# Kernel tuning notes

Measured on AMD Instinct MI355X. Metric: run time of the kernel, lower is better.

The kernel has to match this reference:

```python
import jax, jax.numpy as jnp
import numpy as np

K = 3          # kernel_size
P = 1          # padding
S = 1          # stride
C_IN = 64
C_OUT = 64


def unfold_patches(t, k=K, p=P, s=S):
    """Replicate-pad then extract kxk patches.
    Input  t: [B, C, H, W]
    Output  : [B, Ho, Wo, C, k*k]  matching torch unfold(2).unfold(3).permute(0,2,3,1,4,5).reshape
    (patch index varies as kh*k + kw)."""
    B, C, H, W = t.shape
    tp = jnp.pad(t, ((0, 0), (0, 0), (p, p), (p, p)), mode='edge')
    Ho = (H + 2 * p - k) // s + 1
    Wo = (W + 2 * p - k) // s + 1
    pats = [tp[:, :, a:a + (Ho - 1) * s + 1:s, b:b + (Wo - 1) * s + 1:s]
            for a in range(k) for b in range(k)]
    y = jnp.stack(pats, axis=-1)          # [B, C, Ho, Wo, k*k]
    return jnp.transpose(y, (0, 2, 3, 1, 4))  # [B, Ho, Wo, C, k*k]


def setup_inputs() -> dict:
    key = jax.random.key(0)
    k1, k2, k3, k4, k5, k6, k7 = jax.random.split(key, 7)
    B, H, W = 4, 128, 128
    feat_in = K * K * C_IN * 2      # 1152
    f1_out = K * K * C_IN           # 576
    f2_out = C_IN * C_OUT           # 4096
    lim1 = 1.0 / np.sqrt(feat_in)
    x = jax.random.normal(k1, (B, C_IN, H, W), dtype=jnp.float32)
    m = jax.random.uniform(k2, (B, C_IN, H, W), dtype=jnp.float32)
    s = jax.random.uniform(k3, (B, C_IN, H, W), dtype=jnp.float32)
    W1 = jax.random.uniform(k4, (feat_in, f1_out), minval=-lim1, maxval=lim1, dtype=jnp.float32)
    b1 = jax.random.uniform(k5, (f1_out,), minval=-lim1, maxval=lim1, dtype=jnp.float32)
    W2 = jax.random.uniform(k6, (feat_in, f2_out), minval=-lim1, maxval=lim1, dtype=jnp.float32)
    b2 = jax.random.uniform(k7, (f2_out,), minval=-lim1, maxval=lim1, dtype=jnp.float32)
    return {"x": x, "m": m, "s": s, "W1": W1, "b1": b1, "W2": W2, "b2": b2}


def reference(x, m, s, W1, b1, W2, b2):
    yp = unfold_patches(x)                              # [B,Ho,Wo,Cin,K2]
    mp = jax.lax.stop_gradient(unfold_patches(m))       # torch no_grad
    sp = jax.lax.stop_gradient(unfold_patches(s))
    B, Ho, Wo = yp.shape[:3]

    feat = jnp.concatenate([yp.reshape(B, Ho, Wo, -1),
                            mp.reshape(B, Ho, Wo, -1)], axis=-1)  # [B,Ho,Wo,2*K2*Cin]
    w1 = (feat @ W1 + b1).reshape(B, Ho, Wo, C_IN, K * K)
    w2 = (feat @ W2 + b2).reshape(B, Ho, Wo, C_IN, C_OUT)

    # y = sum_c (sum_k yp*w1) * w2
    yr = jnp.einsum('bhwck,bhwck->bhwc', yp, w1)
    y = jnp.einsum('bhwc,bhwco->bhwo', yr, w2)
    y = jnp.transpose(y, (0, 3, 1, 2))                  # [B,Cout,Ho,Wo]

    aw1 = jnp.abs(w1)
    aw2 = jnp.abs(w2)
    mr = jnp.einsum('bhwck,bhwck->bhwc', mp, aw1)
    m_y = jnp.transpose(jnp.einsum('bhwc,bhwco->bhwo', mr, aw2), (0, 3, 1, 2))
    sr = jnp.einsum('bhwck,bhwck->bhwc', sp, aw1)
    s_y = jnp.transpose(jnp.einsum('bhwc,bhwco->bhwo', sr, aw2), (0, 3, 1, 2))
    m_y = jax.lax.stop_gradient(m_y / s_y)

    return (y, m_y, jnp.ones_like(m_y))
```

## Files before the change

### kernel.cpp

```cpp
#include <hip/hip_runtime.h>
#include <stdint.h>
#include <stddef.h>


using short8   = __attribute__((ext_vector_type(8))) short;
using float4v  = __attribute__((ext_vector_type(4))) float;
using ushort4v = __attribute__((ext_vector_type(4))) unsigned short;

#define DI __device__ __forceinline__

DI unsigned short f2bf(float f) {
  union { float f; unsigned int u; } a; a.f = f;
  unsigned int r = a.u + 0x7fffu + ((a.u >> 16) & 1u);
  return (unsigned short)(r >> 16);
}
DI float bf2f(unsigned short u) {
  union { unsigned int u; float f; } a; a.u = ((unsigned int)u) << 16;
  return a.f;
}
DI void gll16(const void* g, void* l) {
  __builtin_amdgcn_global_load_lds(
      (const __attribute__((address_space(1))) unsigned int*)g,
      (__attribute__((address_space(3))) unsigned int*)l, 16, 0, 0);
}

__global__ void k_feat(const float* __restrict__ x, const float* __restrict__ m,
                       unsigned short* __restrict__ featb) {
  unsigned int tid = blockIdx.x * 256u + threadIdx.x;
  int j8   = tid & 7;
  int pl   = (tid >> 3) & 127;
  int q    = (tid >> 10) & 3;
  int pblk = (tid >> 12) & 511;
  int kk   = tid >> 21;
  int col  = kk * 32 + q * 8 + j8;
  const float* src = x;
  int jx = col;
  if (col >= 576) { src = m; jx = col - 576; }
  int c  = jx / 9;
  int t  = jx - c * 9;
  int t3 = t / 3;
  int dh = t3 - 1;
  int dw = (t - t3 * 3) - 1;
  int p  = pblk * 128 + pl;
  int b  = p >> 14, h = (p >> 7) & 127, w = p & 127;
  int hh = min(max(h + dh, 0), 127);
  int ww = min(max(w + dw, 0), 127);
  featb[tid] = f2bf(src[(((b << 6) | c) << 14) + (hh << 7) + ww]);
}

__global__ void k_sw(const float* __restrict__ Wsrc, unsigned short* __restrict__ Wdst,
                     int ncols, int ntiles, int total, int perm) {
  int tid = blockIdx.x * 256 + threadIdx.x;
  if (tid >= total) return;
  int k = tid / ncols;
  int n = tid - k * ncols;
  int np = perm ? (((n & 63) << 6) | (n >> 6)) : n;
  int out = ((k >> 5) * ntiles + (np >> 4)) * 512 + ((k >> 3) & 3) * 128 +
            (np & 15) * 8 + (k & 7);
  Wdst[out] = f2bf(Wsrc[tid]);
}

__launch_bounds__(512, 2)
__global__ void k_gemm1(const unsigned short* __restrict__ featb,
                        const unsigned short* __restrict__ W1s,
                        const float* __restrict__ b1,
                        const float* __restrict__ x, const float* __restrict__ m,
                        const float* __restrict__ s,
                        float* __restrict__ yr, float* __restrict__ mr,
                        float* __restrict__ sr) {
  __shared__ __align__(16) unsigned short Alds[4096];
  __shared__ __align__(16) unsigned short Blds[4608];
  __shared__ __align__(16) unsigned short w1buf[128 * 152];
  const int tid = threadIdx.x;
  const int wv  = tid >> 6;
  const int l15 = tid & 15;
  const int q   = (tid >> 4) & 3;
  const int bm  = blockIdx.x, nb = blockIdx.y;

  float4v acc[9];
#pragma unroll
  for (int t = 0; t < 9; ++t) acc[t] = (float4v){0.f, 0.f, 0.f, 0.f};

  const unsigned short* Ab = featb + (size_t)bm * 4096;
  const unsigned short* Bb = W1s + (size_t)nb * 9 * 512;

  for (int kk = 0; kk < 36; ++kk) {
    __syncthreads();
    gll16(Ab + (size_t)kk * 2097152 + tid * 8, (char*)Alds + wv * 1024);
    gll16(Bb + (size_t)kk * 18432 + tid * 8, (char*)Blds + wv * 1024);
    if (tid < 64) gll16(Bb + (size_t)kk * 18432 + 4096 + tid * 8, (char*)Blds + 8192);
    __syncthreads();
    short8 af = *(const short8*)&Alds[q * 1024 + (16 * wv + l15) * 8];
#pragma unroll
    for (int t = 0; t < 9; ++t) {
      short8 bfr = *(const short8*)&Blds[t * 512 + q * 128 + l15 * 8];
      acc[t] = __builtin_amdgcn_mfma_f32_16x16x32_bf16(af, bfr, acc[t], 0, 0, 0);
    }
  }

#pragma unroll
  for (int t = 0; t < 9; ++t) {
    int col = 16 * t + l15;
    float bb = b1[nb * 144 + col];
#pragma unroll
    for (int i = 0; i < 4; ++i) {
      int plr = 16 * wv + 4 * q + i;
      w1buf[plr * 152 + col] = f2bf(acc[t][i] + bb);
    }
  }
  __syncthreads();

  const int b = bm >> 7, h = bm & 127;
#pragma unroll
  for (int ii = 0; ii < 4; ++ii) {
    int task = ii * 512 + tid;
    int p  = task >> 4;
    int cl = task & 15;
    int c  = nb * 16 + cl;
    float w1v[9];
#pragma unroll
    for (int k = 0; k < 9; ++k) w1v[k] = bf2f(w1buf[p * 152 + cl * 9 + k]);
    size_t base = (size_t)(((b << 6) | c) << 14);
    float vy = 0.f, vm = 0.f, vs = 0.f;
#pragma unroll
    for (int dh = -1; dh <= 1; ++dh) {
      int hh = min(max(h + dh, 0), 127);
#pragma unroll
      for (int dw = -1; dw <= 1; ++dw) {
        int ww = min(max(p + dw, 0), 127);
        size_t idx = base + (hh << 7) + ww;
        int k = (dh + 1) * 3 + (dw + 1);
        float wv1 = w1v[k], aw = fabsf(wv1);
        vy += x[idx] * wv1;
        vm += m[idx] * aw;
        vs += s[idx] * aw;
      }
    }
    size_t P = (size_t)bm * 128 + p;
    yr[P * 64 + c] = vy;
    mr[P * 64 + c] = vm;
    sr[P * 64 + c] = vs;
  }
}

__launch_bounds__(512, 2)
__global__ void k_gemm2(const unsigned short* __restrict__ featb,
                        const unsigned short* __restrict__ W2s,
                        const float* __restrict__ b2,
                        const float* __restrict__ yr, const float* __restrict__ mr,
                        const float* __restrict__ sr,
                        float* __restrict__ out) {
  __shared__ __align__(16) unsigned short U[3][16384];
  __shared__ __align__(16) unsigned short w2buf[256 * 68];
  const int tid  = threadIdx.x;
  const int wv   = tid >> 6;
  const int lane = tid & 63;
  const int wm   = wv >> 2;
  const int wn   = wv & 3;
  const int l15  = tid & 15;
  const int q    = (tid >> 4) & 3;
  const int part = lane >> 4;
  const int bm   = blockIdx.x;

  const unsigned short* Ab = featb + (size_t)bm * 8192;

  float4v acc[8][4];
#pragma unroll
  for (int r = 0; r < 8; ++r)
#pragma unroll
    for (int t = 0; t < 4; ++t) acc[r][t] = (float4v){0.f, 0.f, 0.f, 0.f};

  gll16(Ab + tid * 8,                  (char*)&U[0][0]     + wv * 1024);
  gll16(Ab + 4096 + tid * 8,           (char*)&U[0][4096]  + wv * 1024);
  gll16(W2s + tid * 8,                 (char*)&U[0][8192]  + wv * 1024);
  gll16(W2s + 4096 + tid * 8,          (char*)&U[0][12288] + wv * 1024);
  gll16(Ab + 2097152 + tid * 8,        (char*)&U[1][0]     + wv * 1024);
  gll16(Ab + 2097152 + 4096 + tid * 8, (char*)&U[1][4096]  + wv * 1024);
  gll16(W2s + 131072 + tid * 8,        (char*)&U[1][8192]  + wv * 1024);
  gll16(W2s + 131072 + 4096 + tid * 8, (char*)&U[1][12288] + wv * 1024);

#define G2_STEP(KK, BR, BS, LAST)                                              \
  do {                                                                         \
    if (LAST) { asm volatile("s_waitcnt vmcnt(0)" ::: "memory"); }             \
    else      { asm volatile("s_waitcnt vmcnt(4)" ::: "memory"); }             \
    __builtin_amdgcn_s_barrier();                                              \
    asm volatile("" ::: "memory");                                             \
    {                                                                          \
      int kks = (KK) + 2, chs = ch;                                            \
      if (kks >= 36) { kks -= 36; chs += 1; }                                  \
      if (chs < 16) {                                                          \
        const unsigned short* Ag = Ab + (size_t)kks * 2097152;                 \
        const unsigned short* Bg = W2s + (size_t)kks * 131072 + chs * 8192;    \
        gll16(Ag + tid * 8,        (char*)&U[BS][0]     + wv * 1024);          \
        gll16(Ag + 4096 + tid * 8, (char*)&U[BS][4096]  + wv * 1024);          \
        gll16(Bg + tid * 8,        (char*)&U[BS][8192]  + wv * 1024);          \
        gll16(Bg + 4096 + tid * 8, (char*)&U[BS][12288] + wv * 1024);          \
      }                                                                        \
    }                                                                          \
    {                                                                          \
      const unsigned short* Al = &U[BR][0];                                    \
      const unsigned short* Bl = &U[BR][8192];                                 \
      short8 a_[8];                                                            \
      _Pragma("unroll") for (int r = 0; r < 8; ++r)                            \
        a_[r] = *(const short8*)&Al[wm * 4096 + q * 1024 + (16 * r + l15) * 8];\
      __builtin_amdgcn_s_setprio(1);                                           \
      _Pragma("unroll") for (int t = 0; t < 4; ++t) {                          \
        short8 bfr = *(const short8*)&Bl[(4 * wn + t) * 512 + q * 128 + l15 * 8]; \
        _Pragma("unroll") for (int r = 0; r < 8; ++r)                          \
          acc[r][t] = __builtin_amdgcn_mfma_f32_16x16x32_bf16(a_[r], bfr,      \
                                                              acc[r][t], 0, 0, 0); \
      }                                                                        \
      __builtin_amdgcn_s_setprio(0);                                           \
    }                                                                          \
  } while (0)

  for (int ch = 0; ch < 16; ++ch) {
    for (int k3 = 0; k3 < 12; ++k3) {
      const int kk = k3 * 3;
      G2_STEP(kk + 0, 0, 2, false);
      G2_STEP(kk + 1, 1, 0, false);
      G2_STEP(kk + 2, 2, 1, (ch == 15 && k3 == 11));
    }

    float b2v[4];
#pragma unroll
    for (int t = 0; t < 4; ++t) b2v[t] = b2[(16 * t + l15) * 64 + 4 * ch + wn];

    for (int p = 0; p < 4; ++p) {
      __syncthreads();
      if (wn == p) {
#pragma unroll
        for (int r = 0; r < 8; ++r)
#pragma unroll
          for (int t = 0; t < 4; ++t)
#pragma unroll
            for (int i = 0; i < 4; ++i)
              w2buf[(128 * wm + 16 * r + 4 * q + i) * 68 + 16 * t + l15] =
                  f2bf(acc[r][t][i] + b2v[t]);
      }
      __syncthreads();
#pragma unroll
      for (int it = 0; it < 2; ++it) {
        const int row = 128 * it + 16 * wv + l15;
        const size_t P = (size_t)bm * 256 + row;
        const float4v* y4 = (const float4v*)(yr + P * 64 + 16 * part);
        const float4v* m4 = (const float4v*)(mr + P * 64 + 16 * part);
        const float4v* s4 = (const float4v*)(sr + P * 64 + 16 * part);
        const ushort4v* w4 = (const ushort4v*)&w2buf[row * 68 + 16 * part];
        float ys = 0.f, ms = 0.f, ss = 0.f;
#pragma unroll
        for (int j4 = 0; j4 < 4; ++j4) {
          float4v yv = y4[j4], mv = m4[j4], sv = s4[j4];
          ushort4v wq = w4[j4];
#pragma unroll
          for (int j = 0; j < 4; ++j) {
            float w2f = bf2f(wq[j]);
            float aw  = fabsf(w2f);
            ys += yv[j] * w2f;
            ms += mv[j] * aw;
            ss += sv[j] * aw;
          }
        }
        ys += __shfl_xor(ys, 16); ys += __shfl_xor(ys, 32);
        ms += __shfl_xor(ms, 16); ms += __shfl_xor(ms, 32);
        ss += __shfl_xor(ss, 16); ss += __shfl_xor(ss, 32);
        if (part == 0) {
          const int o = 4 * ch + p;
          const int b = (int)(P >> 14), h = (int)((P >> 7) & 127), w = (int)(P & 127);
          size_t idx = ((size_t)((b << 6) | o) << 14) + (h << 7) + w;
          out[idx]           = ys;
          out[4194304 + idx] = ms / ss;
          out[8388608 + idx] = 1.0f;
        }
      }
    }
#pragma unroll
    for (int r = 0; r < 8; ++r)
#pragma unroll
      for (int t = 0; t < 4; ++t) acc[r][t] = (float4v){0.f, 0.f, 0.f, 0.f};
  }
#undef G2_STEP
}

extern "C" void kernel_launch(void* const* d_in, const int* in_sizes, int n_in,
                              void* d_out, int out_size, void* d_ws, size_t ws_size,
                              hipStream_t stream) {
  const float* x  = (const float*)d_in[0];
  const float* m  = (const float*)d_in[1];
  const float* s  = (const float*)d_in[2];
  const float* W1 = (const float*)d_in[3];
  const float* b1 = (const float*)d_in[4];
  const float* W2 = (const float*)d_in[5];
  const float* b2 = (const float*)d_in[6];
  float* out = (float*)d_out;

  if (ws_size < 212090880ull) return;
  char* ws = (char*)d_ws;
  unsigned short* featb = (unsigned short*)ws;
  unsigned short* W1s   = (unsigned short*)(ws + 150994944);
  unsigned short* W2s   = (unsigned short*)(ws + 152322048);
  float* yr = (float*)(ws + 161759232);
  float* mr = (float*)(ws + 178536448);
  float* sr = (float*)(ws + 195313664);

  k_feat<<<294912, 256, 0, stream>>>(x, m, featb);
  k_sw<<<2592, 256, 0, stream>>>(W1, W1s, 576, 36, 663552, 0);
  k_sw<<<18432, 256, 0, stream>>>(W2, W2s, 4096, 256, 4718592, 1);
  dim3 g1(512, 4);
  k_gemm1<<<g1, 512, 0, stream>>>(featb, W1s, b1, x, m, s, yr, mr, sr);
  k_gemm2<<<256, 512, 0, stream>>>(featb, W2s, b2, yr, mr, sr, out);
}
```

Measured before the change: 1.316 ms.

## Split each K-step into two half-MFMA phases interleaved with split global-to-LDS prefetches

Restructures the triple-buffered MFMA main loop so each K step runs in two phases. Each phase computes half the A rows with MFMAs, and the A and B prefetches for a later stage are issued separately between the phases. LDS reads are issued before a barrier and waited on with explicit lgkmcnt and sched_barrier, so the compute is fenced from the loads. The aim is to overlap LDS reads and global-to-LDS copies with MFMA work in a ping-pong style schedule. In exchange it adds twice as many barriers per step, and the vmcnt accounting has changed, which could be fragile near the drain at the end.

```diff
diff --git a/kernel.cpp b/kernel.cpp
--- a/kernel.cpp
+++ b/kernel.cpp
@@ -178,48 +178,69 @@
   gll16(Ab + 2097152 + 4096 + tid * 8, (char*)&U[1][4096]  + wv * 1024);
   gll16(W2s + 131072 + tid * 8,        (char*)&U[1][8192]  + wv * 1024);
   gll16(W2s + 131072 + 4096 + tid * 8, (char*)&U[1][12288] + wv * 1024);
-
-#define G2_STEP(KK, BR, BS, LAST)                                              \
+  asm volatile("s_waitcnt vmcnt(4)" ::: "memory");
+  __builtin_amdgcn_s_barrier();
+
+#define G2_KK(KK, BR, BS, DRAIN)                                               \
   do {                                                                         \
-    if (LAST) { asm volatile("s_waitcnt vmcnt(0)" ::: "memory"); }             \
-    else      { asm volatile("s_waitcnt vmcnt(4)" ::: "memory"); }             \
+    const unsigned short* Al = &U[BR][0];                                      \
+    const unsigned short* Bl = &U[BR][8192];                                   \
+    int kks = (KK) + 2, chs = ch;                                              \
+    if (kks >= 36) { kks -= 36; chs += 1; }                                    \
+    const unsigned short* Ag = Ab + (size_t)kks * 2097152;                     \
+    const unsigned short* Bg = W2s + (size_t)kks * 131072 + (size_t)chs * 8192;\
+                           \
+    short8 a0_[4], b_[4];                                                      \
+    _Pragma("unroll") for (int r = 0; r < 4; ++r)                              \
+      a0_[r] = *(const short8*)&Al[wm * 4096 + q * 1024 + r * 128 + l15 * 8];  \
+    _Pragma("unroll") for (int t = 0; t < 4; ++t)                              \
+      b_[t] = *(const short8*)&Bl[(4 * wn + t) * 512 + q * 128 + l15 * 8];     \
+    if (chs < 16) {                                                            \
+      gll16(Ag + tid * 8,        (char*)&U[BS][0]    + wv * 1024);             \
+      gll16(Ag + 4096 + tid * 8, (char*)&U[BS][4096] + wv * 1024);             \
+    }                                                                          \
+    asm volatile("" ::: "memory");                                             \
     __builtin_amdgcn_s_barrier();                                              \
+    asm volatile("s_waitcnt lgkmcnt(0)" ::: "memory");                         \
+    __builtin_amdgcn_sched_barrier(0);                                         \
+    __builtin_amdgcn_s_setprio(1);                                             \
+    _Pragma("unroll") for (int t = 0; t < 4; ++t)                              \
+      _Pragma("unroll") for (int r = 0; r < 4; ++r)                            \
+        acc[r][t] = __builtin_amdgcn_mfma_f32_16x16x32_bf16(a0_[r], b_[t],     \
+                                                            acc[r][t], 0, 0, 0);\
+    __builtin_amdgcn_s_setprio(0);                                             \
     asm volatile("" ::: "memory");                                             \
-    {                                                                          \
-      int kks = (KK) + 2, chs = ch;                                            \
-      if (kks >= 36) { kks -= 36; chs += 1; }                                  \
-      if (chs < 16) {                                                          \
-        const unsigned short* Ag = Ab + (size_t)kks * 2097152;                 \
-        const unsigned short* Bg = W2s + (size_t)kks * 131072 + chs * 8192;    \
-        gll16(Ag + tid * 8,        (char*)&U[BS][0]     + wv * 1024);          \
-        gll16(Ag + 4096 + tid * 8, (char*)&U[BS][4096]  + wv * 1024);          \
-        gll16(Bg + tid * 8,        (char*)&U[BS][8192]  + wv * 1024);          \
-        gll16(Bg + 4096 + tid * 8, (char*)&U[BS][12288] + wv * 1024);          \
-      }                                                                        \
+    __builtin_amdgcn_s_barrier();                                              \
+                    \
+    short8 a1_[4];                                                             \
+    _Pragma("unroll") for (int r = 0; r < 4; ++r)                              \
+      a1_[r] = *(const short8*)&Al[wm * 4096 + q * 1024 + 512 + r * 128 + l15 * 8];\
+    if (chs < 16) {                                                            \
+      gll16(Bg + tid * 8,        (char*)&U[BS][8192]  + wv * 1024);            \
+      gll16(Bg + 4096 + tid * 8, (char*)&U[BS][12288] + wv * 1024);            \
     }                                                                          \
-    {                                                                          \
-      const unsigned short* Al = &U[BR][0];                                    \
-      const unsigned short* Bl = &U[BR][8192];                                 \
-      short8 a_[8];                                                            \
-      _Pragma("unroll") for (int r = 0; r < 8; ++r)                            \
-        a_[r] = *(const short8*)&Al[wm * 4096 + q * 1024 + (16 * r + l15) * 8];\
-      __builtin_amdgcn_s_setprio(1);                                           \
-      _Pragma("unroll") for (int t = 0; t < 4; ++t) {                          \
-        short8 bfr = *(const short8*)&Bl[(4 * wn + t) * 512 + q * 128 + l15 * 8]; \
-        _Pragma("unroll") for (int r = 0; r < 8; ++r)                          \
-          acc[r][t] = __builtin_amdgcn_mfma_f32_16x16x32_bf16(a_[r], bfr,      \
-                                                              acc[r][t], 0, 0, 0); \
-      }                                                                        \
-      __builtin_amdgcn_s_setprio(0);                                           \
-    }                                                                          \
+    if (DRAIN) { asm volatile("s_waitcnt vmcnt(0)" ::: "memory"); }            \
+    else       { asm volatile("s_waitcnt vmcnt(4)" ::: "memory"); }            \
+    __builtin_amdgcn_s_barrier();                                              \
+    asm volatile("s_waitcnt lgkmcnt(0)" ::: "memory");                         \
+    __builtin_amdgcn_sched_barrier(0);                                         \
+    __builtin_amdgcn_s_setprio(1);                                             \
+    _Pragma("unroll") for (int t = 0; t < 4; ++t)                              \
+      _Pragma("unroll") for (int r = 0; r < 4; ++r)                            \
+        acc[4 + r][t] = __builtin_amdgcn_mfma_f32_16x16x32_bf16(a1_[r], b_[t], \
+                                                            acc[4 + r][t], 0, 0, 0);\
+    __builtin_amdgcn_s_setprio(0);                                             \
+    asm volatile("" ::: "memory");                                             \
+    __builtin_amdgcn_s_barrier();                                              \
   } while (0)
 
   for (int ch = 0; ch < 16; ++ch) {
+    const bool lc = (ch == 15);
     for (int k3 = 0; k3 < 12; ++k3) {
       const int kk = k3 * 3;
-      G2_STEP(kk + 0, 0, 2, false);
-      G2_STEP(kk + 1, 1, 0, false);
-      G2_STEP(kk + 2, 2, 1, (ch == 15 && k3 == 11));
+      G2_KK(kk + 0, 0, 2, false);
+      G2_KK(kk + 1, 1, 0, (lc && k3 == 11));
+      G2_KK(kk + 2, 2, 1, (lc && k3 == 11));
     }
 
     float b2v[4];
@@ -279,7 +300,7 @@
 #pragma unroll
       for (int t = 0; t < 4; ++t) acc[r][t] = (float4v){0.f, 0.f, 0.f, 0.f};
   }
-#undef G2_STEP
+#undef G2_KK
 }
 
 extern "C" void kernel_launch(void* const* d_in, const int* in_sizes, int n_in,
```

New measurement: 1.390 ms. 5.6% more time.
